# Kernel tuning notes

Measured on AMD Instinct MI355X. Metric: run time of the kernel, lower is better.

Reference implementation:

```python
import jax, jax.numpy as jnp
import numpy as np

B, C, H, W = 8, 256, 128, 128
CQ = C // 32


def setup_inputs() -> dict:
    key = jax.random.key(0)
    ks = jax.random.split(key, 7)
    return {
        "x": jax.random.normal(ks[0], (B, C, H, W), dtype=jnp.float32),
        "Wq": jax.random.normal(ks[1], (CQ, C), dtype=jnp.float32) * 0.05,
        "bq": jax.random.normal(ks[2], (CQ,), dtype=jnp.float32) * 0.05,
        "Wk": jax.random.normal(ks[3], (CQ, C), dtype=jnp.float32) * 0.05,
        "bk": jax.random.normal(ks[4], (CQ,), dtype=jnp.float32) * 0.05,
        "Wv": jax.random.normal(ks[5], (C, C), dtype=jnp.float32) * 0.05,
        "bv": jax.random.normal(ks[6], (C,), dtype=jnp.float32) * 0.05,
        "gamma": jnp.zeros((1,), dtype=jnp.float32),
    }


def reference(x, Wq, bq, Wk, bk, Wv, bv, gamma):
    b, c, h, w = x.shape
    # scale = max(1, int(sqrt(H*W/1024))) -- static given static shapes
    scale = max(1, int((h * w / 1024) ** 0.5))
    hd, wd = h // scale, w // scale
    # avg_pool2d(kernel=stride=scale); H,W divisible by scale here
    x_down = x.reshape(b, c, hd, scale, wd, scale).mean(axis=(3, 5))  # [B,C,Hd,Wd]
    xf = x_down.reshape(b, c, hd * wd)  # [B,C,N]
    # 1x1 convs == per-pixel GEMMs
    q = jnp.einsum('oc,bcn->bon', Wq, xf) + bq[None, :, None]  # [B,Cq,N]
    k = jnp.einsum('oc,bcn->bon', Wk, xf) + bk[None, :, None]  # [B,Cq,N]
    v = jnp.einsum('oc,bcn->bon', Wv, xf) + bv[None, :, None]  # [B,C,N]
    # attention[b,m,n] = softmax_n(q[b,:,m] . k[b,:,n])
    attn = jax.nn.softmax(jnp.einsum('bcm,bcn->bmn', q, k), axis=-1)  # [B,N,N]
    out = jnp.einsum('bcn,bmn->bcm', v, attn).reshape(b, c, hd, wd)
    if hd != h or wd != w:
        # bilinear, align_corners=False == half-pixel centers (jax.image default)
        out = jax.image.resize(out, (b, c, h, w), method='linear')
    return gamma * out + x
```

## Files before the change

kernel.cpp:

```cpp
#include <hip/hip_runtime.h>
#include <hip/hip_bf16.h>


typedef short bf16x8 __attribute__((ext_vector_type(8)));
typedef float f32x4 __attribute__((ext_vector_type(4)));
typedef unsigned short ushort_t;

__device__ __forceinline__ ushort_t f2bf(float f) {
    union { float f; unsigned u; } x{f};
    unsigned r = x.u + 0x7FFF + ((x.u >> 16) & 1);
    return (ushort_t)(r >> 16);
}
__device__ __forceinline__ float bf2f(ushort_t u) {
    return __uint_as_float(((unsigned)u) << 16);
}

#define GLOAD_LDS16(gp, lp)                                                          \
    __builtin_amdgcn_global_load_lds((const __attribute__((address_space(1))) void*)(gp), \
                                     (__attribute__((address_space(3))) void*)(lp), 16, 0, 0)


__global__ __launch_bounds__(256) void pool_kernel(const float* __restrict__ x,
                                                   float* __restrict__ xf) {
    int idx = blockIdx.x * 256 + threadIdx.x;
    int n = idx & 1023;
    int c = (idx >> 10) & 255;
    int b = idx >> 18;
    int hi = n >> 5, wi = n & 31;
    const float* p = x + ((size_t)(b * 256 + c) * 128 + hi * 4) * 128 + wi * 4;
    float s = 0.f;
#pragma unroll
    for (int r = 0; r < 4; ++r) {
        float4 v4 = *(const float4*)(p + r * 128);
        s += v4.x + v4.y + v4.z + v4.w;
    }
    xf[idx] = s * 0.0625f;
}

__global__ __launch_bounds__(256) void qk_kernel(const float* __restrict__ xf,
                                                 const float* __restrict__ Wq,
                                                 const float* __restrict__ bq,
                                                 const float* __restrict__ Wk,
                                                 const float* __restrict__ bk,
                                                 float* __restrict__ qT,
                                                 float* __restrict__ kT) {
    __shared__ float sW[4112];
    __shared__ float red[4352];
    int t = threadIdx.x;
    for (int i = t; i < 2048; i += 256) {
        sW[i] = Wq[i];
        sW[2048 + i] = Wk[i];
    }
    if (t < 8) { sW[4096 + t] = bq[t]; sW[4104 + t] = bk[t]; }
    __syncthreads();

    int b = blockIdx.x >> 5;
    int ng = blockIdx.x & 31;
    int nl = t & 31, cg = t >> 5;
    float a[16];
#pragma unroll
    for (int j = 0; j < 16; ++j) a[j] = 0.f;
    const float* xp = xf + (size_t)b * 262144 + ng * 32 + nl;
    for (int c = cg * 32; c < cg * 32 + 32; ++c) {
        float xv = xp[(size_t)c * 1024];
#pragma unroll
        for (int j = 0; j < 8; ++j) {
            a[j]     = fmaf(sW[j * 256 + c], xv, a[j]);
            a[8 + j] = fmaf(sW[2048 + j * 256 + c], xv, a[8 + j]);
        }
    }
    float* rp = &red[cg * 544 + nl * 17];
#pragma unroll
    for (int j = 0; j < 16; ++j) rp[j] = a[j];
    __syncthreads();
#pragma unroll
    for (int u = 0; u < 2; ++u) {
        int o = t * 2 + u;
        int n = o >> 4, j = o & 15;
        float s = sW[4096 + j];
#pragma unroll
        for (int g = 0; g < 8; ++g) s += red[g * 544 + n * 17 + j];
        if (j < 8) qT[((size_t)b * 1024 + ng * 32 + n) * 8 + j] = s;
        else       kT[((size_t)b * 1024 + ng * 32 + n) * 8 + j - 8] = s;
    }
}

__global__ __launch_bounds__(256) void vgemm_kernel(const float* __restrict__ xf,
                                                    const float* __restrict__ Wv,
                                                    const float* __restrict__ bv,
                                                    ushort_t* __restrict__ v) {
    int bid = blockIdx.x;
    int b = bid >> 6;
    int ot0 = ((bid >> 4) & 3) * 64;
    int nt0 = (bid & 15) * 64;
    __shared__ float WsT[32][64];
    __shared__ float Xs[32][64];
    int t = threadIdx.x;
    int to4 = (t >> 4) * 4, tn4 = (t & 15) * 4;
    float acc[4][4] = {};

    for (int c0 = 0; c0 < 256; c0 += 32) {
        {
            int o = t >> 2, ck0 = (t & 3) * 8;
            const float* wp = Wv + (size_t)(ot0 + o) * 256 + c0 + ck0;
            float4 aa = *(const float4*)wp;
            float4 bb = *(const float4*)(wp + 4);
            WsT[ck0 + 0][o] = aa.x;  WsT[ck0 + 1][o] = aa.y;
            WsT[ck0 + 2][o] = aa.z;  WsT[ck0 + 3][o] = aa.w;
            WsT[ck0 + 4][o] = bb.x; WsT[ck0 + 5][o] = bb.y;
            WsT[ck0 + 6][o] = bb.z; WsT[ck0 + 7][o] = bb.w;
        }
        {
            int c = t >> 3, nch = (t & 7) * 8;
            const float* xp = xf + (size_t)(b * 256 + c0 + c) * 1024 + nt0 + nch;
            *(float4*)&Xs[c][nch] = *(const float4*)xp;
            *(float4*)&Xs[c][nch + 4] = *(const float4*)(xp + 4);
        }
        __syncthreads();
#pragma unroll
        for (int ck = 0; ck < 32; ++ck) {
            float4 wv = *(float4*)&WsT[ck][to4];
            float4 xv = *(float4*)&Xs[ck][tn4];
            float wr[4] = {wv.x, wv.y, wv.z, wv.w};
            float xr[4] = {xv.x, xv.y, xv.z, xv.w};
#pragma unroll
            for (int i = 0; i < 4; ++i)
#pragma unroll
                for (int j = 0; j < 4; ++j)
                    acc[i][j] = fmaf(wr[i], xr[j], acc[i][j]);
        }
        __syncthreads();
    }
#pragma unroll
    for (int i = 0; i < 4; ++i) {
        float bias = bv[ot0 + to4 + i];
        ushort4 r;
        r.x = f2bf(acc[i][0] + bias); r.y = f2bf(acc[i][1] + bias);
        r.z = f2bf(acc[i][2] + bias); r.w = f2bf(acc[i][3] + bias);
        *(ushort4*)&v[(size_t)(b * 256 + ot0 + to4 + i) * 1024 + nt0 + tn4] = r;
    }
}

__global__ __launch_bounds__(256) void pmat_kernel(const float* __restrict__ qT,
                                                   const float* __restrict__ kT,
                                                   ushort_t* __restrict__ Pm) {
    __shared__ float4 kst[2048];
    int t = threadIdx.x;
    int b = blockIdx.x >> 6;
    int mg = blockIdx.x & 63;
    const float* kp = kT + (size_t)b * 8192;
    for (int i4 = t * 4; i4 < 8192; i4 += 1024) {
        float4 kv = *(const float4*)&kp[i4];
        int n = i4 >> 3;
        int h = (i4 >> 2) & 1;
        kst[h * 1024 + n] = kv;
    }
    __syncthreads();

    int w = t >> 6, ln = t & 63;
#pragma unroll 1
    for (int pass = 0; pass < 4; ++pass) {
        int m = mg * 16 + pass * 4 + w;
        const float* qp = qT + ((size_t)b * 1024 + m) * 8;
        float4 q0 = *(const float4*)qp, q1 = *(const float4*)(qp + 4);
        float s[16];
        float mx = -1e30f;
#pragma unroll
        for (int i = 0; i < 16; ++i) {
            float4 k0 = kst[ln + i * 64];
            float4 k1 = kst[1024 + ln + i * 64];
            float d = q0.x * k0.x + q0.y * k0.y + q0.z * k0.z + q0.w * k0.w +
                      q1.x * k1.x + q1.y * k1.y + q1.z * k1.z + q1.w * k1.w;
            s[i] = d;
            mx = fmaxf(mx, d);
        }
#pragma unroll
        for (int off = 32; off; off >>= 1) mx = fmaxf(mx, __shfl_xor(mx, off, 64));
        float sum = 0.f;
#pragma unroll
        for (int i = 0; i < 16; ++i) { s[i] = __expf(s[i] - mx); sum += s[i]; }
#pragma unroll
        for (int off = 32; off; off >>= 1) sum += __shfl_xor(sum, off, 64);
        float inv = 1.0f / sum;
        ushort_t* pp = Pm + ((size_t)b * 1024 + m) * 1024;
#pragma unroll
        for (int i = 0; i < 16; ++i) pp[ln + i * 64] = f2bf(s[i] * inv);
    }
}

__global__ __launch_bounds__(256) void pv_mfma_kernel(const ushort_t* __restrict__ v,
                                                      const ushort_t* __restrict__ Pm,
                                                      ushort_t* __restrict__ outs) {
    int bid = blockIdx.x;
    int b = bid >> 6;
    int ct0 = ((bid >> 4) & 3) * 64;
    int mt0 = (bid & 15) * 64;
    __shared__ __align__(16) short vs[4096];
    __shared__ __align__(16) short ps[4096];
    int t = threadIdx.x;
    int w = t >> 6, ln = t & 63;
    int lrow = ln >> 3, lcol = ln & 7;
    int scol = lcol ^ lrow;

    const char* vg = (const char*)(v + (size_t)(b * 256 + ct0) * 1024);
    const char* pg = (const char*)(Pm + (size_t)(b * 1024 + mt0) * 1024);

    f32x4 acc[4] = {};
    int fr = ln & 15, quad = ln >> 4;
    int f7 = fr & 7;

    for (int n0 = 0; n0 < 1024; n0 += 64) {
        __syncthreads();
#pragma unroll
        for (int s = w; s < 8; s += 4) {
            GLOAD_LDS16(vg + (size_t)(s * 8 + lrow) * 2048 + n0 * 2 + scol * 16,
                        (char*)vs + s * 1024);
            GLOAD_LDS16(pg + (size_t)(s * 8 + lrow) * 2048 + n0 * 2 + scol * 16,
                        (char*)ps + s * 1024);
        }
        __syncthreads();
        const char* vb = (const char*)vs + (w * 16 + fr) * 128;
        const char* pb = (const char*)ps;
#pragma unroll
        for (int kh = 0; kh < 2; ++kh) {
            int cb = ((kh * 4 + quad) ^ f7) * 16;
            bf16x8 af = *(const bf16x8*)(vb + cb);
#pragma unroll
            for (int mt = 0; mt < 4; ++mt) {
                bf16x8 bfr = *(const bf16x8*)(pb + (mt * 16 + fr) * 128 + cb);
                acc[mt] = __builtin_amdgcn_mfma_f32_16x16x32_bf16(af, bfr, acc[mt], 0, 0, 0);
            }
        }
    }
    ushort_t* og = outs + (size_t)(b * 256 + ct0 + w * 16) * 1024 + mt0;
#pragma unroll
    for (int mt = 0; mt < 4; ++mt) {
#pragma unroll
        for (int r = 0; r < 4; ++r) {
            int c = quad * 4 + r;
            og[(size_t)c * 1024 + mt * 16 + fr] = f2bf(acc[mt][r]);
        }
    }
}

__global__ __launch_bounds__(256) void up_kernel(const ushort_t* __restrict__ outs,
                                                 const float* __restrict__ x,
                                                 const float* __restrict__ gamma,
                                                 float* __restrict__ out) {
    int bc = blockIdx.x;
    __shared__ float P[32][33];
    __shared__ float R[128][33];
    int t = threadIdx.x;
    const ushort_t* sp = outs + (size_t)bc * 1024;
    for (int i = t; i < 1024; i += 256) P[i >> 5][i & 31] = bf2f(sp[i]);
    float g = gamma[0];
    __syncthreads();

    {
        int wq = t & 31;
        int hbase = (t >> 5) * 16;
#pragma unroll
        for (int hh = 0; hh < 16; ++hh) {
            int h = hbase + hh;
            int hq = h >> 2, r = h & 3;
            int i0 = hq + ((r < 2) ? -1 : 0);
            float fh = (r < 2) ? (0.625f + 0.25f * r) : (0.25f * r - 0.375f);
            int ha = i0 < 0 ? 0 : i0;
            int hb = (i0 + 1) > 31 ? 31 : (i0 + 1);
            R[h][wq] = (1.f - fh) * P[ha][wq] + fh * P[hb][wq];
        }
    }
    __syncthreads();

    const float* xp = x + (size_t)bc * 16384;
    float* op = out + (size_t)bc * 16384;
#pragma unroll 1
    for (int it = 0; it < 16; ++it) {
        int pix = it * 256 + t;
        int h = pix >> 5;
        int wq = pix & 31;
        float4 xv = *(const float4*)(xp + h * 128 + wq * 4);
        float res[4];
#pragma unroll
        for (int k = 0; k < 4; ++k) {
            int j0 = wq + ((k < 2) ? -1 : 0);
            float fw = (k < 2) ? (0.625f + 0.25f * k) : (0.25f * k - 0.375f);
            int wa = j0 < 0 ? 0 : j0;
            int wb = (j0 + 1) > 31 ? 31 : (j0 + 1);
            res[k] = (1.f - fw) * R[h][wa] + fw * R[h][wb];
        }
        f32x4 o;
        o[0] = fmaf(g, res[0], xv.x);
        o[1] = fmaf(g, res[1], xv.y);
        o[2] = fmaf(g, res[2], xv.z);
        o[3] = fmaf(g, res[3], xv.w);
        __builtin_nontemporal_store(o, (f32x4*)(op + h * 128 + wq * 4));
    }
}

extern "C" void kernel_launch(void* const* d_in, const int* in_sizes, int n_in,
                              void* d_out, int out_size, void* d_ws, size_t ws_size,
                              hipStream_t stream) {
    const float* x     = (const float*)d_in[0];
    const float* Wq    = (const float*)d_in[1];
    const float* bq    = (const float*)d_in[2];
    const float* Wk    = (const float*)d_in[3];
    const float* bk    = (const float*)d_in[4];
    const float* Wv    = (const float*)d_in[5];
    const float* bv    = (const float*)d_in[6];
    const float* gamma = (const float*)d_in[7];
    float* out = (float*)d_out;

    char* wsb = (char*)d_ws;
    float*    xf   = (float*)wsb;
    ushort_t* Pmat = (ushort_t*)wsb;
    float*    qT   = (float*)(wsb + 16777216);
    float*    kT   = (float*)(wsb + 17039360);
    ushort_t* v    = (ushort_t*)(wsb + 17301504);
    ushort_t* outs = (ushort_t*)(wsb + 21495808);

    pool_kernel<<<8192, 256, 0, stream>>>(x, xf);
    qk_kernel<<<256, 256, 0, stream>>>(xf, Wq, bq, Wk, bk, qT, kT);
    vgemm_kernel<<<512, 256, 0, stream>>>(xf, Wv, bv, v);
    pmat_kernel<<<512, 256, 0, stream>>>(qT, kT, Pmat);
    pv_mfma_kernel<<<512, 256, 0, stream>>>(v, Pmat, outs);
    up_kernel<<<2048, 256, 0, stream>>>(outs, x, gamma, out);
}
```

Before: 318.4 us.

## Move V projection to bf16 MFMA and double-buffer PV loads

Adds a prep kernel that converts Wv to bf16 and transposes the pooled input into a bf16 [N,C] layout. The V projection then runs on MFMA with async global-to-LDS loads instead of a scalar fp32 FMA GEMM. The PV kernel gains double-buffered LDS stages so the next tile loads while the current one computes. This costs an extra launch, more workspace and lower-precision V inputs.

```diff
diff --git a/kernel.cpp b/kernel.cpp
--- a/kernel.cpp
+++ b/kernel.cpp
@@ -37,6 +37,57 @@
     xf[idx] = s * 0.0625f;
 }
 
+__global__ __launch_bounds__(256) void prep_kernel(const float* __restrict__ xf,
+                                                   const float* __restrict__ Wv,
+                                                   ushort_t* __restrict__ xfT,
+                                                   ushort_t* __restrict__ wvb) {
+    int bid = blockIdx.x;
+    int t = threadIdx.x;
+    if (bid >= 128) {
+        int base = (bid - 128) * 8192 + t * 8;
+#pragma unroll
+        for (int u = 0; u < 8192; u += 2048) {
+            float4 a = *(const float4*)(Wv + base + u);
+            float4 c4 = *(const float4*)(Wv + base + u + 4);
+            bf16x8 r;
+            r[0] = (short)f2bf(a.x);  r[1] = (short)f2bf(a.y);
+            r[2] = (short)f2bf(a.z);  r[3] = (short)f2bf(a.w);
+            r[4] = (short)f2bf(c4.x); r[5] = (short)f2bf(c4.y);
+            r[6] = (short)f2bf(c4.z); r[7] = (short)f2bf(c4.w);
+            *(bf16x8*)(wvb + base + u) = r;
+        }
+        return;
+    }
+    int b = bid >> 4;
+    int n0 = (bid & 15) * 64;
+    __shared__ float tile[64][68];
+    const float* xp = xf + (size_t)b * 262144;
+#pragma unroll 1
+    for (int c0 = 0; c0 < 256; c0 += 64) {
+        {
+            int c = t >> 2, nq = (t & 3) * 16;
+            const float* p = xp + (size_t)(c0 + c) * 1024 + n0 + nq;
+            *(float4*)&tile[c][nq]      = *(const float4*)p;
+            *(float4*)&tile[c][nq + 4]  = *(const float4*)(p + 4);
+            *(float4*)&tile[c][nq + 8]  = *(const float4*)(p + 8);
+            *(float4*)&tile[c][nq + 12] = *(const float4*)(p + 12);
+        }
+        __syncthreads();
+        {
+            int n = t >> 2, cq = (t & 3) * 16;
+            ushort_t* op = xfT + ((size_t)b * 1024 + n0 + n) * 256 + c0 + cq;
+            bf16x8 v0, v1;
+#pragma unroll
+            for (int u = 0; u < 8; ++u) v0[u] = (short)f2bf(tile[cq + u][n]);
+#pragma unroll
+            for (int u = 0; u < 8; ++u) v1[u] = (short)f2bf(tile[cq + 8 + u][n]);
+            *(bf16x8*)op = v0;
+            *(bf16x8*)(op + 8) = v1;
+        }
+        __syncthreads();
+    }
+}
+
 __global__ __launch_bounds__(256) void qk_kernel(const float* __restrict__ xf,
                                                  const float* __restrict__ Wq,
                                                  const float* __restrict__ bq,
@@ -85,59 +136,69 @@
     }
 }
 
-__global__ __launch_bounds__(256) void vgemm_kernel(const float* __restrict__ xf,
-                                                    const float* __restrict__ Wv,
+__global__ __launch_bounds__(256) void vgemm_kernel(const ushort_t* __restrict__ wvb,
+                                                    const ushort_t* __restrict__ xfT,
                                                     const float* __restrict__ bv,
                                                     ushort_t* __restrict__ v) {
     int bid = blockIdx.x;
     int b = bid >> 6;
     int ot0 = ((bid >> 4) & 3) * 64;
     int nt0 = (bid & 15) * 64;
-    __shared__ float WsT[32][64];
-    __shared__ float Xs[32][64];
-    int t = threadIdx.x;
-    int to4 = (t >> 4) * 4, tn4 = (t & 15) * 4;
-    float acc[4][4] = {};
-
-    for (int c0 = 0; c0 < 256; c0 += 32) {
-        {
-            int o = t >> 2, ck0 = (t & 3) * 8;
-            const float* wp = Wv + (size_t)(ot0 + o) * 256 + c0 + ck0;
-            float4 aa = *(const float4*)wp;
-            float4 bb = *(const float4*)(wp + 4);
-            WsT[ck0 + 0][o] = aa.x;  WsT[ck0 + 1][o] = aa.y;
-            WsT[ck0 + 2][o] = aa.z;  WsT[ck0 + 3][o] = aa.w;
-            WsT[ck0 + 4][o] = bb.x; WsT[ck0 + 5][o] = bb.y;
-            WsT[ck0 + 6][o] = bb.z; WsT[ck0 + 7][o] = bb.w;
-        }
-        {
-            int c = t >> 3, nch = (t & 7) * 8;
-            const float* xp = xf + (size_t)(b * 256 + c0 + c) * 1024 + nt0 + nch;
-            *(float4*)&Xs[c][nch] = *(const float4*)xp;
-            *(float4*)&Xs[c][nch + 4] = *(const float4*)(xp + 4);
+    __shared__ __align__(16) short as_[2][4096];
+    __shared__ __align__(16) short bs_[2][4096];
+    int t = threadIdx.x;
+    int w = t >> 6, ln = t & 63;
+    int lrow = ln >> 3, lcol = ln & 7;
+    int scol = lcol ^ lrow;
+
+    const char* ag = (const char*)(wvb + (size_t)ot0 * 256);
+    const char* bg = (const char*)(xfT + ((size_t)b * 1024 + nt0) * 256);
+
+    f32x4 acc[4] = {};
+    int fr = ln & 15, quad = ln >> 4;
+    int f7 = fr & 7;
+
+#define VG_STAGE(bb, koff)                                                        \
+    {                                                                             \
+        _Pragma("unroll")                                                         \
+        for (int s = w; s < 8; s += 4) {                                          \
+            GLOAD_LDS16(ag + (size_t)(s * 8 + lrow) * 512 + (koff) + scol * 16,   \
+                        (char*)as_[bb] + s * 1024);                               \
+            GLOAD_LDS16(bg + (size_t)(s * 8 + lrow) * 512 + (koff) + scol * 16,   \
+                        (char*)bs_[bb] + s * 1024);                               \
+        }                                                                         \
+    }
+
+    VG_STAGE(0, 0);
+    __syncthreads();
+#pragma unroll 1
+    for (int it = 0; it < 4; ++it) {
+        int cur = it & 1;
+        if (it < 3) VG_STAGE(cur ^ 1, (it + 1) * 128);
+        const char* ab = (const char*)as_[cur] + (w * 16 + fr) * 128;
+        const char* bb2 = (const char*)bs_[cur];
+#pragma unroll
+        for (int kh = 0; kh < 2; ++kh) {
+            int cb = ((kh * 4 + quad) ^ f7) * 16;
+            bf16x8 af = *(const bf16x8*)(ab + cb);
+#pragma unroll
+            for (int mt = 0; mt < 4; ++mt) {
+                bf16x8 bfr = *(const bf16x8*)(bb2 + (mt * 16 + fr) * 128 + cb);
+                acc[mt] = __builtin_amdgcn_mfma_f32_16x16x32_bf16(af, bfr, acc[mt], 0, 0, 0);
+            }
         }
         __syncthreads();
-#pragma unroll
-        for (int ck = 0; ck < 32; ++ck) {
-            float4 wv = *(float4*)&WsT[ck][to4];
-            float4 xv = *(float4*)&Xs[ck][tn4];
-            float wr[4] = {wv.x, wv.y, wv.z, wv.w};
-            float xr[4] = {xv.x, xv.y, xv.z, xv.w};
-#pragma unroll
-            for (int i = 0; i < 4; ++i)
-#pragma unroll
-                for (int j = 0; j < 4; ++j)
-                    acc[i][j] = fmaf(wr[i], xr[j], acc[i][j]);
-        }
-        __syncthreads();
-    }
-#pragma unroll
-    for (int i = 0; i < 4; ++i) {
-        float bias = bv[ot0 + to4 + i];
-        ushort4 r;
-        r.x = f2bf(acc[i][0] + bias); r.y = f2bf(acc[i][1] + bias);
-        r.z = f2bf(acc[i][2] + bias); r.w = f2bf(acc[i][3] + bias);
-        *(ushort4*)&v[(size_t)(b * 256 + ot0 + to4 + i) * 1024 + nt0 + tn4] = r;
+    }
+#undef VG_STAGE
+    ushort_t* og = v + (size_t)(b * 256 + ot0 + w * 16) * 1024 + nt0;
+#pragma unroll
+    for (int mt = 0; mt < 4; ++mt) {
+#pragma unroll
+        for (int r = 0; r < 4; ++r) {
+            int o = quad * 4 + r;
+            float bias = bv[ot0 + w * 16 + o];
+            og[(size_t)o * 1024 + mt * 16 + fr] = f2bf(acc[mt][r] + bias);
+        }
     }
 }
 
@@ -195,8 +256,8 @@
     int b = bid >> 6;
     int ct0 = ((bid >> 4) & 3) * 64;
     int mt0 = (bid & 15) * 64;
-    __shared__ __align__(16) short vs[4096];
-    __shared__ __align__(16) short ps[4096];
+    __shared__ __align__(16) short vs[2][4096];
+    __shared__ __align__(16) short ps[2][4096];
     int t = threadIdx.x;
     int w = t >> 6, ln = t & 63;
     int lrow = ln >> 3, lcol = ln & 7;
@@ -209,18 +270,25 @@
     int fr = ln & 15, quad = ln >> 4;
     int f7 = fr & 7;
 
-    for (int n0 = 0; n0 < 1024; n0 += 64) {
-        __syncthreads();
-#pragma unroll
-        for (int s = w; s < 8; s += 4) {
-            GLOAD_LDS16(vg + (size_t)(s * 8 + lrow) * 2048 + n0 * 2 + scol * 16,
-                        (char*)vs + s * 1024);
-            GLOAD_LDS16(pg + (size_t)(s * 8 + lrow) * 2048 + n0 * 2 + scol * 16,
-                        (char*)ps + s * 1024);
-        }
-        __syncthreads();
-        const char* vb = (const char*)vs + (w * 16 + fr) * 128;
-        const char* pb = (const char*)ps;
+#define PV_STAGE(bb, koff)                                                        \
+    {                                                                             \
+        _Pragma("unroll")                                                         \
+        for (int s = w; s < 8; s += 4) {                                          \
+            GLOAD_LDS16(vg + (size_t)(s * 8 + lrow) * 2048 + (koff) + scol * 16,  \
+                        (char*)vs[bb] + s * 1024);                                \
+            GLOAD_LDS16(pg + (size_t)(s * 8 + lrow) * 2048 + (koff) + scol * 16,  \
+                        (char*)ps[bb] + s * 1024);                                \
+        }                                                                         \
+    }
+
+    PV_STAGE(0, 0);
+    __syncthreads();
+#pragma unroll 1
+    for (int it = 0; it < 16; ++it) {
+        int cur = it & 1;
+        if (it < 15) PV_STAGE(cur ^ 1, (it + 1) * 128);
+        const char* vb = (const char*)vs[cur] + (w * 16 + fr) * 128;
+        const char* pb = (const char*)ps[cur];
 #pragma unroll
         for (int kh = 0; kh < 2; ++kh) {
             int cb = ((kh * 4 + quad) ^ f7) * 16;
@@ -231,7 +299,9 @@
                 acc[mt] = __builtin_amdgcn_mfma_f32_16x16x32_bf16(af, bfr, acc[mt], 0, 0, 0);
             }
         }
-    }
+        __syncthreads();
+    }
+#undef PV_STAGE
     ushort_t* og = outs + (size_t)(b * 256 + ct0 + w * 16) * 1024 + mt0;
 #pragma unroll
     for (int mt = 0; mt < 4; ++mt) {
@@ -318,10 +388,13 @@
     float*    kT   = (float*)(wsb + 17039360);
     ushort_t* v    = (ushort_t*)(wsb + 17301504);
     ushort_t* outs = (ushort_t*)(wsb + 21495808);
+    ushort_t* xfT  = (ushort_t*)(wsb + 25690112);
+    ushort_t* wvb  = (ushort_t*)(wsb + 29884416);
 
     pool_kernel<<<8192, 256, 0, stream>>>(x, xf);
+    prep_kernel<<<136, 256, 0, stream>>>(xf, Wv, xfT, wvb);
     qk_kernel<<<256, 256, 0, stream>>>(xf, Wq, bq, Wk, bk, qT, kT);
-    vgemm_kernel<<<512, 256, 0, stream>>>(xf, Wv, bv, v);
+    vgemm_kernel<<<512, 256, 0, stream>>>(wvb, xfT, bv, v);
     pmat_kernel<<<512, 256, 0, stream>>>(qT, kT, Pmat);
     pv_mfma_kernel<<<512, 256, 0, stream>>>(v, Pmat, outs);
     up_kernel<<<2048, 256, 0, stream>>>(outs, x, gamma, out);
```

Result: slower. 344.1 us (+8.1%).
